# Optimization experiments

Measured on AMD Instinct MI355X. Metric: run time of the kernel, lower is better.

## Reference

```python
import jax, jax.numpy as jnp
from jax import lax
import numpy as np

B, T, I, H, O = 64, 4096, 128, 256, 1

def setup_inputs() -> dict:
    key = jax.random.key(0)
    ks = jax.random.split(key, 6)
    x = jax.random.normal(ks[0], (B, T, I), dtype=jnp.float32)
    # Linear params with torch-style fan_in init scale
    Wd = jax.random.uniform(ks[1], (H, I), jnp.float32, -1.0, 1.0) / np.sqrt(I)
    bd = jax.random.uniform(ks[2], (H,), jnp.float32, -1.0, 1.0) / np.sqrt(I)
    Wo = jax.random.uniform(ks[3], (O, H), jnp.float32, -1.0, 1.0) / np.sqrt(H)
    bo = jax.random.uniform(ks[4], (O,), jnp.float32, -1.0, 1.0) / np.sqrt(H)
    tau = jnp.ones((H,), jnp.float32) * 2.0
    return {"x": x, "Wd": Wd, "bd": bd, "Wo": Wo, "bo": bo, "tau": tau}

def reference(x, Wd, bd, Wo, bo, tau):
    # precompute dense projection for all timesteps: [B,T,H]
    cur = jnp.einsum('bti,hi->bth', x, Wd) + bd
    alpha = jax.nn.sigmoid(tau)  # [H], per-channel decay
    mem0 = jnp.zeros((x.shape[0], tau.shape[0]), dtype=x.dtype)

    def step(mem, c_t):  # c_t: [B,H]
        mem = alpha * mem + (1.0 - alpha) * c_t
        return mem, mem

    _, mems = lax.scan(step, mem0, jnp.swapaxes(cur, 0, 1))  # mems: [T,B,H]
    mems = jnp.swapaxes(mems, 0, 1)  # [B,T,H]
    out = jax.nn.sigmoid(jnp.einsum('bth,oh->bto', mems, Wo) + bo)  # [B,T,O]
    return out
```

## Files before the change

### kernel.cpp

```cpp
#include <hip/hip_runtime.h>
#include <hip/hip_bf16.h>
#include <math.h>

#define BB 64
#define TT 4096
#define II 128
#define HH 256
#define DD 64
#define LL 128
#define WR 192
#define NC (TT/LL)

typedef __attribute__((ext_vector_type(8))) short short8;
typedef __attribute__((ext_vector_type(4))) float f32x4;

__device__ inline ushort f2b(float f) {
    __hip_bfloat16 h = __float2bfloat16(f);
    return *reinterpret_cast<ushort*>(&h);
}

__global__ __launch_bounds__(256) void k0_tables(
    const float* __restrict__ Wd, const float* __restrict__ bd,
    const float* __restrict__ Wo, const float* __restrict__ bo,
    const float* __restrict__ tau,
    ushort* __restrict__ U, float* __restrict__ ybias)
{
    __shared__ float la[HH], wg[HH], wb[HH];
    const int tid = threadIdx.x;
    {
        float a = 1.0f / (1.0f + expf(-tau[tid]));
        la[tid] = log2f(a);
        wg[tid] = Wo[tid] * (1.0f - a);
        wb[tid] = Wo[tid] * bd[tid];
    }
    __syncthreads();
    const int idx = blockIdx.x * 256 + tid;
    const int d = idx >> 7, i = idx & 127;
    float s = 0.0f;
    for (int h = 0; h < HH; ++h)
        s += wg[h] * exp2f((float)d * la[h]) * Wd[h * II + i];
    U[idx] = f2b(s);
    if (blockIdx.x == 0 && tid < LL) {
        float yb = bo[0];
        for (int h = 0; h < HH; ++h)
            yb += wb[h] * (1.0f - exp2f((float)(tid + 1) * la[h]));
        ybias[tid] = yb;
    }
}

__global__ __launch_bounds__(512, 6) void k1_conv(
    const float* __restrict__ x, const ushort* __restrict__ U,
    const float* __restrict__ ybias, float* __restrict__ out)
{
    __shared__ __align__(16) char smem[51456];
    float* P    = reinterpret_cast<float*>(smem);
    float* psum = reinterpret_cast<float*>(smem + 49920);

    const int blk = (blockIdx.x & 7) * 256 + (blockIdx.x >> 3);
    const int b = blk >> 5, tc = blk & 31;
    const int t0 = tc * LL;
    const int tid  = threadIdx.x;
    const int lane = tid & 63, w = tid >> 6;
    const int l15  = lane & 15, quad = lane >> 4;

#pragma unroll
    for (int it = 0; it < 6; ++it) {
        int c = it * 512 + tid;
        int r = c >> 4, ib = c & 15;
        int s = t0 - (DD - 1) + r;
        short8 pk = {0, 0, 0, 0, 0, 0, 0, 0};
        if (s >= 0 && s < TT) {
            const float4* src = reinterpret_cast<const float4*>(
                x + ((size_t)b * TT + s) * II + ib * 8);
            float4 v0 = src[0], v1 = src[1];
            ushort* pu = reinterpret_cast<ushort*>(&pk);
            pu[0] = f2b(v0.x); pu[1] = f2b(v0.y); pu[2] = f2b(v0.z); pu[3] = f2b(v0.w);
            pu[4] = f2b(v1.x); pu[5] = f2b(v1.y); pu[6] = f2b(v1.z); pu[7] = f2b(v1.w);
        }
        int byte = (r << 8) + (ib << 4);
        byte ^= (r & 7) << 4;
        *reinterpret_cast<short8*>(smem + byte) = pk;
    }
    __syncthreads();

    const int nt = w & 3, mg = w >> 2;
    f32x4 acc[6];
#pragma unroll
    for (int m = 0; m < 6; ++m) acc[m] = (f32x4){0.f, 0.f, 0.f, 0.f};
#pragma unroll
    for (int kt = 0; kt < 4; ++kt) {
        short8 bfrag = *reinterpret_cast<const short8*>(
            &U[(nt * 16 + l15) * II + kt * 32 + quad * 8]);
#pragma unroll
        for (int m = 0; m < 6; ++m) {
            int row  = (mg * 6 + m) * 16 + l15;
            int byte = (row << 8) + kt * 64 + quad * 16;
            byte ^= (row & 7) << 4;
            short8 afrag = *reinterpret_cast<const short8*>(smem + byte);
            acc[m] = __builtin_amdgcn_mfma_f32_16x16x32_bf16(afrag, bfrag, acc[m], 0, 0, 0);
        }
    }
    __syncthreads();

#pragma unroll
    for (int m = 0; m < 6; ++m)
#pragma unroll
        for (int rr = 0; rr < 4; ++rr)
            P[((mg * 6 + m) * 16 + quad * 4 + rr) * 65 + nt * 16 + l15] = acc[m][rr];
    __syncthreads();

    const int k = tid & 127, g = tid >> 7;
    float part = 0.0f;
#pragma unroll
    for (int i = 0; i < 16; ++i) {
        int d = g * 16 + i;
        part += P[(k + (DD - 1) - d) * 65 + d];
    }
    if (g) psum[(g - 1) * 128 + k] = part;
    __syncthreads();
    if (tid < 128) {
        float y = part + psum[k] + psum[128 + k] + psum[256 + k];
        int t = t0 + k;
        float yb = ybias[t < 128 ? t : 127];
        out[(size_t)b * TT + t] = 1.0f / (1.0f + expf(-(y + yb)));
    }
}

extern "C" void kernel_launch(void* const* d_in, const int* in_sizes, int n_in,
                              void* d_out, int out_size, void* d_ws, size_t ws_size,
                              hipStream_t stream) {
    const float* x   = (const float*)d_in[0];
    const float* Wd  = (const float*)d_in[1];
    const float* bd  = (const float*)d_in[2];
    const float* Wo  = (const float*)d_in[3];
    const float* bo  = (const float*)d_in[4];
    const float* tau = (const float*)d_in[5];
    float* out = (float*)d_out;

    float* ws = (float*)d_ws;
    float*  ybias = ws;
    ushort* U     = (ushort*)(ws + 128);

    k0_tables<<<32, 256, 0, stream>>>(Wd, bd, Wo, bo, tau, U, ybias);
    k1_conv<<<BB * NC, 512, 0, stream>>>(x, U, ybias, out);
}
```

Baseline: 229.1 us.

## Drop halo reload in conv kernel; combine chunk-boundary partial sums in a fixup pass

Each conv block now loads only its own 128 timesteps of x rather than 128+63 halo rows, and computes full-convolution outputs over 192 positions. Edge contributions that spill into the next chunk, or are missing from the previous one, are written to workspace buffers and combined by a new small k2_out kernel. The table-building kernel is also re-parallelised across 72 blocks, with ybias computed by a shuffle reduction. This reduces redundant x reads and shared memory (allowing higher occupancy) at the cost of an extra launch and small workspace traffic.

```diff
diff --git a/kernel.cpp b/kernel.cpp
--- a/kernel.cpp
+++ b/kernel.cpp
@@ -8,7 +8,6 @@
 #define HH 256
 #define DD 64
 #define LL 128
-#define WR 192
 #define NC (TT/LL)
 
 typedef __attribute__((ext_vector_type(8))) short short8;
@@ -25,58 +24,77 @@
     const float* __restrict__ tau,
     ushort* __restrict__ U, float* __restrict__ ybias)
 {
-    __shared__ float la[HH], wg[HH], wb[HH];
+    __shared__ float pw[HH];
+    __shared__ float wb[HH];
+    __shared__ float red[II];
     const int tid = threadIdx.x;
-    {
-        float a = 1.0f / (1.0f + expf(-tau[tid]));
-        la[tid] = log2f(a);
-        wg[tid] = Wo[tid] * (1.0f - a);
-        wb[tid] = Wo[tid] * bd[tid];
-    }
-    __syncthreads();
-    const int idx = blockIdx.x * 256 + tid;
-    const int d = idx >> 7, i = idx & 127;
-    float s = 0.0f;
-    for (int h = 0; h < HH; ++h)
-        s += wg[h] * exp2f((float)d * la[h]) * Wd[h * II + i];
-    U[idx] = f2b(s);
-    if (blockIdx.x == 0 && tid < LL) {
-        float yb = bo[0];
-        for (int h = 0; h < HH; ++h)
-            yb += wb[h] * (1.0f - exp2f((float)(tid + 1) * la[h]));
-        ybias[tid] = yb;
+    const int blk = blockIdx.x;
+
+    if (blk < DD) {
+        const int d = blk;
+        {
+            float a = 1.0f / (1.0f + expf(-tau[tid]));
+            pw[tid] = Wo[tid] * (1.0f - a) * exp2f((float)d * log2f(a));
+        }
+        __syncthreads();
+        const int i = tid & 127, p = tid >> 7;
+        float s = 0.0f;
+#pragma unroll 8
+        for (int hh = 0; hh < 128; ++hh) {
+            int h = p * 128 + hh;
+            s += pw[h] * Wd[h * II + i];
+        }
+        if (p) red[i] = s;
+        __syncthreads();
+        if (!p) U[d * II + i] = f2b(s + red[i]);
+    } else {
+        {
+            float a = 1.0f / (1.0f + expf(-tau[tid]));
+            pw[tid] = log2f(a);
+            wb[tid] = Wo[tid] * bd[tid];
+        }
+        __syncthreads();
+        const int t = (blk - DD) * 16 + (tid >> 4);
+        const int hp = tid & 15;
+        float s = 0.0f;
+#pragma unroll
+        for (int hh = 0; hh < 16; ++hh) {
+            int h = hp * 16 + hh;
+            s += wb[h] * (1.0f - exp2f((float)(t + 1) * pw[h]));
+        }
+#pragma unroll
+        for (int m = 1; m < 16; m <<= 1) s += __shfl_xor(s, m, 64);
+        if (hp == 0) ybias[t] = s + bo[0];
     }
 }
 
-__global__ __launch_bounds__(512, 6) void k1_conv(
+__global__ __launch_bounds__(512, 8) void k1_conv(
     const float* __restrict__ x, const ushort* __restrict__ U,
-    const float* __restrict__ ybias, float* __restrict__ out)
+    const float* __restrict__ ybias,
+    float* __restrict__ fix, float* __restrict__ spill,
+    float* __restrict__ out)
 {
-    __shared__ __align__(16) char smem[51456];
+    __shared__ __align__(16) char smem[34048];
     float* P    = reinterpret_cast<float*>(smem);
-    float* psum = reinterpret_cast<float*>(smem + 49920);
+    float* psum = reinterpret_cast<float*>(smem + 33280);
 
-    const int blk = (blockIdx.x & 7) * 256 + (blockIdx.x >> 3);
-    const int b = blk >> 5, tc = blk & 31;
+    const int b = blockIdx.x >> 5, tc = blockIdx.x & 31;
     const int t0 = tc * LL;
     const int tid  = threadIdx.x;
     const int lane = tid & 63, w = tid >> 6;
     const int l15  = lane & 15, quad = lane >> 4;
 
+    const float4* xg = reinterpret_cast<const float4*>(x + ((size_t)b * TT + t0) * II);
 #pragma unroll
-    for (int it = 0; it < 6; ++it) {
+    for (int it = 0; it < 4; ++it) {
         int c = it * 512 + tid;
         int r = c >> 4, ib = c & 15;
-        int s = t0 - (DD - 1) + r;
-        short8 pk = {0, 0, 0, 0, 0, 0, 0, 0};
-        if (s >= 0 && s < TT) {
-            const float4* src = reinterpret_cast<const float4*>(
-                x + ((size_t)b * TT + s) * II + ib * 8);
-            float4 v0 = src[0], v1 = src[1];
-            ushort* pu = reinterpret_cast<ushort*>(&pk);
-            pu[0] = f2b(v0.x); pu[1] = f2b(v0.y); pu[2] = f2b(v0.z); pu[3] = f2b(v0.w);
-            pu[4] = f2b(v1.x); pu[5] = f2b(v1.y); pu[6] = f2b(v1.z); pu[7] = f2b(v1.w);
-        }
+        float4 v0 = xg[r * 32 + ib * 2];
+        float4 v1 = xg[r * 32 + ib * 2 + 1];
+        short8 pk;
+        ushort* pu = reinterpret_cast<ushort*>(&pk);
+        pu[0] = f2b(v0.x); pu[1] = f2b(v0.y); pu[2] = f2b(v0.z); pu[3] = f2b(v0.w);
+        pu[4] = f2b(v1.x); pu[5] = f2b(v1.y); pu[6] = f2b(v1.z); pu[7] = f2b(v1.w);
         int byte = (r << 8) + (ib << 4);
         byte ^= (r & 7) << 4;
         *reinterpret_cast<short8*>(smem + byte) = pk;
@@ -84,46 +102,72 @@
     __syncthreads();
 
     const int nt = w & 3, mg = w >> 2;
-    f32x4 acc[6];
+    f32x4 acc[4];
 #pragma unroll
-    for (int m = 0; m < 6; ++m) acc[m] = (f32x4){0.f, 0.f, 0.f, 0.f};
+    for (int mi = 0; mi < 4; ++mi) acc[mi] = (f32x4){0.f, 0.f, 0.f, 0.f};
 #pragma unroll
     for (int kt = 0; kt < 4; ++kt) {
         short8 bfrag = *reinterpret_cast<const short8*>(
             &U[(nt * 16 + l15) * II + kt * 32 + quad * 8]);
 #pragma unroll
-        for (int m = 0; m < 6; ++m) {
-            int row  = (mg * 6 + m) * 16 + l15;
+        for (int mi = 0; mi < 4; ++mi) {
+            int row  = (mg * 4 + mi) * 16 + l15;
             int byte = (row << 8) + kt * 64 + quad * 16;
             byte ^= (row & 7) << 4;
             short8 afrag = *reinterpret_cast<const short8*>(smem + byte);
-            acc[m] = __builtin_amdgcn_mfma_f32_16x16x32_bf16(afrag, bfrag, acc[m], 0, 0, 0);
+            acc[mi] = __builtin_amdgcn_mfma_f32_16x16x32_bf16(afrag, bfrag, acc[mi], 0, 0, 0);
         }
     }
     __syncthreads();
 
 #pragma unroll
-    for (int m = 0; m < 6; ++m)
+    for (int mi = 0; mi < 4; ++mi)
 #pragma unroll
         for (int rr = 0; rr < 4; ++rr)
-            P[((mg * 6 + m) * 16 + quad * 4 + rr) * 65 + nt * 16 + l15] = acc[m][rr];
+            P[((mg * 4 + mi) * 16 + quad * 4 + rr) * 65 + nt * 16 + l15] = acc[mi][rr];
     __syncthreads();
 
-    const int k = tid & 127, g = tid >> 7;
+    const int g = tid >> 8;
+    const int j = tid & 255;
     float part = 0.0f;
+    if (j < 192) {
 #pragma unroll
-    for (int i = 0; i < 16; ++i) {
-        int d = g * 16 + i;
-        part += P[(k + (DD - 1) - d) * 65 + d];
+        for (int i = 0; i < 32; ++i) {
+            int d = g * 32 + i;
+            int r = j - d;
+            int rc = r < 0 ? 0 : (r > 127 ? 127 : r);
+            float v = P[rc * 65 + d];
+            part += (r == rc) ? v : 0.0f;
+        }
+        if (g) psum[j] = part;
     }
-    if (g) psum[(g - 1) * 128 + k] = part;
     __syncthreads();
-    if (tid < 128) {
-        float y = part + psum[k] + psum[128 + k] + psum[256 + k];
-        int t = t0 + k;
-        float yb = ybias[t < 128 ? t : 127];
-        out[(size_t)b * TT + t] = 1.0f / (1.0f + expf(-(y + yb)));
+    if (!g && j < 192) {
+        float tot = part + psum[j];
+        if (j < 63) {
+            fix[((size_t)b * NC + tc) * 64 + j] = tot;
+        } else if (j < 128) {
+            int t = t0 + j;
+            float yb = ybias[t < 128 ? t : 127];
+            out[(size_t)b * TT + t] = 1.0f / (1.0f + expf(-(tot + yb)));
+        } else {
+            spill[((size_t)b * NC + tc) * 64 + (j - 128)] = tot;
+        }
     }
+}
+
+__global__ __launch_bounds__(256) void k2_out(
+    const float* __restrict__ fix, const float* __restrict__ spill,
+    const float* __restrict__ ybias, float* __restrict__ out)
+{
+    int idx = blockIdx.x * 256 + threadIdx.x;
+    int j = idx & 63, tc = (idx >> 6) & 31, b = idx >> 11;
+    if (j >= 63) return;
+    float v = fix[((size_t)b * NC + tc) * 64 + j];
+    if (tc) v += spill[((size_t)b * NC + tc - 1) * 64 + j];
+    int t = tc * LL + j;
+    v += ybias[t < 128 ? t : 127];
+    out[(size_t)b * TT + t] = 1.0f / (1.0f + expf(-v));
 }
 
 extern "C" void kernel_launch(void* const* d_in, const int* in_sizes, int n_in,
@@ -140,7 +184,10 @@
     float* ws = (float*)d_ws;
     float*  ybias = ws;
     ushort* U     = (ushort*)(ws + 128);
+    float*  fix   = ws + 128 + 4096;
+    float*  spill = fix + BB * NC * 64;
 
-    k0_tables<<<32, 256, 0, stream>>>(Wd, bd, Wo, bo, tau, U, ybias);
-    k1_conv<<<BB * NC, 512, 0, stream>>>(x, U, ybias, out);
+    k0_tables<<<72, 256, 0, stream>>>(Wd, bd, Wo, bo, tau, U, ybias);
+    k1_conv<<<BB * NC, 512, 0, stream>>>(x, U, ybias, fix, spill, out);
+    k2_out<<<512, 256, 0, stream>>>(fix, spill, ybias, out);
 }
```

Result: faster. 213.6 us (-6.8%).
